# Kernel tuning notes

Measured on AMD Instinct MI355X. Metric: run time of the kernel, lower is better.

The kernel has to match this reference:

```python
import jax, jax.numpy as jnp
import numpy as np


def setup_inputs() -> dict:
    key = jax.random.key(0)
    k1, k2, k3, k4, k5 = jax.random.split(key, 5)
    B, D, T = 32, 256, 32       # batch, word_feature_dim, seq_len
    Dh, H, Wd = 128, 128, 128   # image_feature_dim, height, width
    word_features = jax.random.normal(k1, (B, D, T), dtype=jnp.float32)
    image_features = jax.random.normal(k2, (B, Dh, H, Wd), dtype=jnp.float32)
    words_mask = jax.random.randint(k3, (B, T), 0, 2, dtype=jnp.int32)
    W = jax.random.normal(k4, (Dh, D), dtype=jnp.float32) * (1.0 / np.sqrt(D))
    b = jax.random.normal(k5, (Dh,), dtype=jnp.float32) * 0.01
    return {"word_features": word_features, "image_features": image_features,
            "words_mask": words_mask, "W": W, "b": b}


def reference(word_features, image_features, words_mask, W, b):
    B, D, T = word_features.shape
    Dh = image_features.shape[1]
    N = image_features.shape[2] * image_features.shape[3]  # H*W
    # values = fc(word_features^T)^T : [B, Dh, T]
    values = jnp.einsum('bdt,kd->bkt', word_features, W) + b[None, :, None]
    # queries: [B, N, Dh] (flatten spatial)
    queries = image_features.reshape(B, Dh, N)
    # scores S: [B, N, T]
    S = jnp.einsum('bkn,bkt->bnt', queries, values)
    mask = (words_mask != 0)[:, None, :]  # [B,1,T], True => masked
    S = jnp.where(mask, -jnp.inf, S)
    # softmax over seq dim (original: exp / sum(exp)); stable form is same math
    attn_coefficients = jax.nn.softmax(S, axis=2)  # [B, N, T]
    # context vectors: [B, Dh, N]
    attn = jnp.einsum('bkt,bnt->bkn', values, attn_coefficients)
    return attn, attn_coefficients
```

## Files before the change

kernel.cpp:

```cpp
#include <hip/hip_runtime.h>
#include <math.h>

constexpr int Bc  = 32;
constexpr int Dc  = 256;
constexpr int Tc  = 32;
constexpr int DHc = 128;
constexpr int Nc  = 16384;

typedef _Float16 v8hf __attribute__((ext_vector_type(8)));
typedef _Float16 v2hf __attribute__((ext_vector_type(2)));
typedef float    v4f  __attribute__((ext_vector_type(4)));

__global__ __launch_bounds__(256) void values_kernel(
    const float* __restrict__ wf, const float* __restrict__ Wm,
    const float* __restrict__ bias, float* __restrict__ values)
{
    int id = blockIdx.x * 256 + threadIdx.x;
    int t = id & (Tc - 1);
    int k = (id >> 5) & (DHc - 1);
    int b = id >> 12;
    const float* wrow = Wm + (size_t)k * Dc;
    const float* wfp  = wf + (size_t)b * Dc * Tc + t;
    float acc = bias[k];
    #pragma unroll 8
    for (int d = 0; d < Dc; ++d)
        acc = fmaf(wrow[d], wfp[(size_t)d * Tc], acc);
    values[id] = acc;
}

__device__ __forceinline__ _Float16 pick_half(int u, int sel) {
    unsigned short s = (unsigned short)(sel ? (u >> 16) : u);
    return __builtin_bit_cast(_Float16, s);
}

__global__ __launch_bounds__(256) void attn_kernel(
    const float* __restrict__ img, const float* __restrict__ values,
    const int* __restrict__ mask, float* __restrict__ attn,
    float* __restrict__ coeff)
{
    constexpr int VT_LD = 136;
    constexpr int VP_LD = 40;
    __shared__ _Float16 VTh[Tc * VT_LD];
    __shared__ _Float16 VTl[Tc * VT_LD];
    __shared__ _Float16 VPh[DHc * VP_LD];
    __shared__ float mneg[Tc];

    const int tid   = threadIdx.x;
    const int b     = blockIdx.x >> 5;
    const int strip = blockIdx.x & 31;

    {
        const float* vb = values + (size_t)b * DHc * Tc;
        #pragma unroll
        for (int i = 0; i < 16; ++i) {
            int idx = tid + 256 * i;
            int k = idx >> 5, t = idx & 31;
            float v = vb[idx];
            _Float16 vh = (_Float16)v;
            _Float16 vl = (_Float16)(v - (float)vh);
            VTh[t * VT_LD + k] = vh;
            VTl[t * VT_LD + k] = vl;
            VPh[k * VP_LD + t] = vh;
        }
        if (tid < Tc) mneg[tid] = mask[b * Tc + tid] ? -INFINITY : 0.0f;
    }
    __syncthreads();

    const int lane = tid & 63;
    const int wave = tid >> 6;
    const int c    = lane & 15;
    const int g    = lane >> 4;

    float madd[2][4];
    #pragma unroll
    for (int tt = 0; tt < 2; ++tt)
        #pragma unroll
        for (int r = 0; r < 4; ++r)
            madd[tt][r] = mneg[16 * tt + 4 * g + r];

    v8hf VB[8];
    #pragma unroll
    for (int mt = 0; mt < 8; ++mt)
        VB[mt] = *(const v8hf*)&VPh[(16 * mt + c) * VP_LD + 8 * g];

    const float* qbase = img  + ((size_t)b * DHc + 8 * g) * Nc + c;
    float*       abase = attn + ((size_t)b * DHc + c) * Nc + 4 * g;
    float*       cbase = coeff + (size_t)b * Nc * Tc;

    const int ls_lo = c + 32 * (g & 1);
    const int sel   = g >> 1;

    for (int it = 0; it < 8; ++it) {
        const int n0 = strip * 512 + (it * 4 + wave) * 16;

        const float* qp = qbase + n0;
        v8hf Qh[4], Ql[4];
        #pragma unroll
        for (int ks = 0; ks < 4; ++ks)
            #pragma unroll
            for (int j = 0; j < 8; ++j) {
                float qv = qp[(size_t)(ks * 32 + j) * Nc];
                _Float16 h = (_Float16)qv;
                Qh[ks][j] = h;
                Ql[ks][j] = (_Float16)(qv - (float)h);
            }

        v4f Sh[2], Sl[2];
        #pragma unroll
        for (int tt = 0; tt < 2; ++tt) {
            Sh[tt] = (v4f){0.f, 0.f, 0.f, 0.f};
            Sl[tt] = (v4f){0.f, 0.f, 0.f, 0.f};
        }
        #pragma unroll
        for (int tt = 0; tt < 2; ++tt) {
            const int rowbase = (16 * tt + c) * VT_LD + 8 * g;
            #pragma unroll
            for (int ks = 0; ks < 4; ++ks) {
                v8hf va = *(const v8hf*)&VTh[rowbase + ks * 32];
                v8hf vl = *(const v8hf*)&VTl[rowbase + ks * 32];
                Sh[tt] = __builtin_amdgcn_mfma_f32_16x16x32_f16(va, Qh[ks], Sh[tt], 0, 0, 0);
                Sl[tt] = __builtin_amdgcn_mfma_f32_16x16x32_f16(va, Ql[ks], Sl[tt], 0, 0, 0);
                Sl[tt] = __builtin_amdgcn_mfma_f32_16x16x32_f16(vl, Qh[ks], Sl[tt], 0, 0, 0);
            }
        }

        float p0[4], p1[4];
        float m = -INFINITY;
        #pragma unroll
        for (int r = 0; r < 4; ++r) {
            p0[r] = Sh[0][r] + Sl[0][r] + madd[0][r];
            p1[r] = Sh[1][r] + Sl[1][r] + madd[1][r];
            m = fmaxf(m, fmaxf(p0[r], p1[r]));
        }
        m = fmaxf(m, __shfl_xor(m, 16));
        m = fmaxf(m, __shfl_xor(m, 32));
        float sum = 0.0f;
        #pragma unroll
        for (int r = 0; r < 4; ++r) {
            p0[r] = __expf(p0[r] - m); sum += p0[r];
            p1[r] = __expf(p1[r] - m); sum += p1[r];
        }
        sum += __shfl_xor(sum, 16);
        sum += __shfl_xor(sum, 32);
        const float inv = 1.0f / sum;
        #pragma unroll
        for (int r = 0; r < 4; ++r) { p0[r] *= inv; p1[r] *= inv; }

        float* cp = cbase + (size_t)(n0 + c) * Tc + 4 * g;
        *(float4*)cp        = make_float4(p0[0], p0[1], p0[2], p0[3]);
        *(float4*)(cp + 16) = make_float4(p1[0], p1[1], p1[2], p1[3]);

        v8hf Pb;
        #pragma unroll
        for (int r = 0; r < 4; ++r) {
            v2hf h2; h2[0] = (_Float16)p0[r]; h2[1] = (_Float16)p1[r];
            int u   = __builtin_bit_cast(int, h2);
            int ulo = __shfl(u, ls_lo);
            int uhi = __shfl(u, ls_lo + 16);
            Pb[r]     = pick_half(ulo, sel);
            Pb[4 + r] = pick_half(uhi, sel);
        }

        #pragma unroll
        for (int mt = 0; mt < 8; ++mt) {
            v4f o = (v4f){0.f, 0.f, 0.f, 0.f};
            o = __builtin_amdgcn_mfma_f32_16x16x32_f16(Pb, VB[mt], o, 0, 0, 0);
            float* ap = abase + (size_t)(16 * mt) * Nc + n0;
            *(float4*)ap = make_float4(o[0], o[1], o[2], o[3]);
        }
    }
}

extern "C" void kernel_launch(void* const* d_in, const int* in_sizes, int n_in,
                              void* d_out, int out_size, void* d_ws, size_t ws_size,
                              hipStream_t stream)
{
    const float* wf   = (const float*)d_in[0];
    const float* img  = (const float*)d_in[1];
    const int*   msk  = (const int*)d_in[2];
    const float* Wm   = (const float*)d_in[3];
    const float* bias = (const float*)d_in[4];

    float* attn  = (float*)d_out;
    float* coeff = attn + (size_t)Bc * DHc * Nc;
    float* vals  = (float*)d_ws;

    values_kernel<<<(Bc * DHc * Tc) / 256, 256, 0, stream>>>(wf, Wm, bias, vals);
    attn_kernel<<<Bc * 32, 256, 0, stream>>>(img, vals, msk, attn, coeff);
}
```

Baseline: 595.3 us.

## Tile values GEMM in LDS, emit fp16 split layouts, prefetch image queries

The values kernel now stages word features and a 16-row slice of W in shared memory. It computes two outputs per thread and writes pre-split fp16 hi/lo transposed and plain layouts straight to the workspace. The attention kernel then loads those with vectorized 16-byte copies instead of converting and transposing on the fly. It also double-buffers the image query loads for the next iteration in registers, sets launch bounds for occupancy of 4, and reads the V operand from LDS per use instead of keeping it in registers. The point is to hide global-load latency and cut the values-kernel cost, at the price of extra register pressure from the prefetch buffers.

```diff
diff --git a/kernel.cpp b/kernel.cpp
--- a/kernel.cpp
+++ b/kernel.cpp
@@ -13,19 +13,63 @@
 
 __global__ __launch_bounds__(256) void values_kernel(
     const float* __restrict__ wf, const float* __restrict__ Wm,
-    const float* __restrict__ bias, float* __restrict__ values)
+    const float* __restrict__ bias,
+    _Float16* __restrict__ vth, _Float16* __restrict__ vtl,
+    _Float16* __restrict__ vph)
 {
-    int id = blockIdx.x * 256 + threadIdx.x;
-    int t = id & (Tc - 1);
-    int k = (id >> 5) & (DHc - 1);
-    int b = id >> 12;
-    const float* wrow = Wm + (size_t)k * Dc;
-    const float* wfp  = wf + (size_t)b * Dc * Tc + t;
-    float acc = bias[k];
-    #pragma unroll 8
-    for (int d = 0; d < Dc; ++d)
-        acc = fmaf(wrow[d], wfp[(size_t)d * Tc], acc);
-    values[id] = acc;
+    __shared__ float wfs[Dc * Tc];
+    __shared__ float Ws[16 * 260];
+
+    const int tid = threadIdx.x;
+    const int b   = blockIdx.x >> 3;
+    const int k0  = (blockIdx.x & 7) * 16;
+
+    {
+        const float4* src = (const float4*)(wf + (size_t)b * Dc * Tc);
+        float4* dst = (float4*)wfs;
+        #pragma unroll
+        for (int i = 0; i < 8; ++i) dst[tid + 256 * i] = src[tid + 256 * i];
+    }
+    {
+        #pragma unroll
+        for (int i = 0; i < 4; ++i) {
+            int f = tid + 256 * i;
+            int row = f >> 6, d4 = f & 63;
+            *(float4*)&Ws[row * 260 + 4 * d4] =
+                *(const float4*)&Wm[(size_t)(k0 + row) * Dc + 4 * d4];
+        }
+    }
+    __syncthreads();
+
+    const int kl  = tid >> 4;
+    const int tt0 = (tid & 15) * 2;
+    const int k   = k0 + kl;
+
+    float acc0 = bias[k], acc1 = acc0;
+    #pragma unroll
+    for (int d4 = 0; d4 < 64; ++d4) {
+        const float4 w4 = *(const float4*)&Ws[kl * 260 + 4 * d4];
+        #pragma unroll
+        for (int j = 0; j < 4; ++j) {
+            const float2 f2 = *(const float2*)&wfs[(4 * d4 + j) * Tc + tt0];
+            const float wv = (j == 0) ? w4.x : (j == 1) ? w4.y : (j == 2) ? w4.z : w4.w;
+            acc0 = fmaf(wv, f2.x, acc0);
+            acc1 = fmaf(wv, f2.y, acc1);
+        }
+    }
+
+    _Float16 vh0 = (_Float16)acc0, vh1 = (_Float16)acc1;
+    _Float16 vl0 = (_Float16)(acc0 - (float)vh0);
+    _Float16 vl1 = (_Float16)(acc1 - (float)vh1);
+
+    {
+        v2hf p; p[0] = vh0; p[1] = vh1;
+        *(v2hf*)&vph[((size_t)b * DHc + k) * Tc + tt0] = p;
+    }
+    vth[((size_t)b * Tc + tt0)     * DHc + k] = vh0;
+    vth[((size_t)b * Tc + tt0 + 1) * DHc + k] = vh1;
+    vtl[((size_t)b * Tc + tt0)     * DHc + k] = vl0;
+    vtl[((size_t)b * Tc + tt0 + 1) * DHc + k] = vl1;
 }
 
 __device__ __forceinline__ _Float16 pick_half(int u, int sel) {
@@ -33,16 +77,18 @@
     return __builtin_bit_cast(_Float16, s);
 }
 
-__global__ __launch_bounds__(256) void attn_kernel(
-    const float* __restrict__ img, const float* __restrict__ values,
+__global__ __launch_bounds__(256, 4) void attn_kernel(
+    const float* __restrict__ img,
+    const _Float16* __restrict__ vth, const _Float16* __restrict__ vtl,
+    const _Float16* __restrict__ vph,
     const int* __restrict__ mask, float* __restrict__ attn,
     float* __restrict__ coeff)
 {
     constexpr int VT_LD = 136;
     constexpr int VP_LD = 40;
-    __shared__ _Float16 VTh[Tc * VT_LD];
-    __shared__ _Float16 VTl[Tc * VT_LD];
-    __shared__ _Float16 VPh[DHc * VP_LD];
+    __shared__ __align__(16) _Float16 VTh[Tc * VT_LD];
+    __shared__ __align__(16) _Float16 VTl[Tc * VT_LD];
+    __shared__ __align__(16) _Float16 VPh[DHc * VP_LD];
     __shared__ float mneg[Tc];
 
     const int tid   = threadIdx.x;
@@ -50,17 +96,17 @@
     const int strip = blockIdx.x & 31;
 
     {
-        const float* vb = values + (size_t)b * DHc * Tc;
-        #pragma unroll
-        for (int i = 0; i < 16; ++i) {
-            int idx = tid + 256 * i;
-            int k = idx >> 5, t = idx & 31;
-            float v = vb[idx];
-            _Float16 vh = (_Float16)v;
-            _Float16 vl = (_Float16)(v - (float)vh);
-            VTh[t * VT_LD + k] = vh;
-            VTl[t * VT_LD + k] = vl;
-            VPh[k * VP_LD + t] = vh;
+        const uint4* sth = (const uint4*)(vth + (size_t)b * Tc * DHc);
+        const uint4* stl = (const uint4*)(vtl + (size_t)b * Tc * DHc);
+        const uint4* sph = (const uint4*)(vph + (size_t)b * DHc * Tc);
+        #pragma unroll
+        for (int i = 0; i < 2; ++i) {
+            int cid = tid + 256 * i;
+            int t = cid >> 4, cc = cid & 15;
+            *(uint4*)&VTh[t * VT_LD + 8 * cc] = sth[cid];
+            *(uint4*)&VTl[t * VT_LD + 8 * cc] = stl[cid];
+            int kk = cid >> 2, c4 = cid & 3;
+            *(uint4*)&VPh[kk * VP_LD + 8 * c4] = sph[cid];
         }
         if (tid < Tc) mneg[tid] = mask[b * Tc + tid] ? -INFINITY : 0.0f;
     }
@@ -78,11 +124,6 @@
         for (int r = 0; r < 4; ++r)
             madd[tt][r] = mneg[16 * tt + 4 * g + r];
 
-    v8hf VB[8];
-    #pragma unroll
-    for (int mt = 0; mt < 8; ++mt)
-        VB[mt] = *(const v8hf*)&VPh[(16 * mt + c) * VP_LD + 8 * g];
-
     const float* qbase = img  + ((size_t)b * DHc + 8 * g) * Nc + c;
     float*       abase = attn + ((size_t)b * DHc + c) * Nc + 4 * g;
     float*       cbase = coeff + (size_t)b * Nc * Tc;
@@ -90,16 +131,31 @@
     const int ls_lo = c + 32 * (g & 1);
     const int sel   = g >> 1;
 
+    float qa[32], qb[32];
+    {
+        const float* qp = qbase + strip * 512 + wave * 16;
+        #pragma unroll
+        for (int u = 0; u < 32; ++u)
+            qa[u] = qp[(size_t)((u >> 3) * 32 + (u & 7)) * Nc];
+    }
+
+    #pragma unroll 2
     for (int it = 0; it < 8; ++it) {
         const int n0 = strip * 512 + (it * 4 + wave) * 16;
 
-        const float* qp = qbase + n0;
+        if (it < 7) {
+            const float* qpn = qbase + n0 + 64;
+            #pragma unroll
+            for (int u = 0; u < 32; ++u)
+                qb[u] = qpn[(size_t)((u >> 3) * 32 + (u & 7)) * Nc];
+        }
+
         v8hf Qh[4], Ql[4];
         #pragma unroll
         for (int ks = 0; ks < 4; ++ks)
             #pragma unroll
             for (int j = 0; j < 8; ++j) {
-                float qv = qp[(size_t)(ks * 32 + j) * Nc];
+                float qv = qa[ks * 8 + j];
                 _Float16 h = (_Float16)qv;
                 Qh[ks][j] = h;
                 Ql[ks][j] = (_Float16)(qv - (float)h);
@@ -163,10 +219,16 @@
 
         #pragma unroll
         for (int mt = 0; mt < 8; ++mt) {
+            v8hf vb2 = *(const v8hf*)&VPh[(16 * mt + c) * VP_LD + 8 * g];
             v4f o = (v4f){0.f, 0.f, 0.f, 0.f};
-            o = __builtin_amdgcn_mfma_f32_16x16x32_f16(Pb, VB[mt], o, 0, 0, 0);
+            o = __builtin_amdgcn_mfma_f32_16x16x32_f16(Pb, vb2, o, 0, 0, 0);
             float* ap = abase + (size_t)(16 * mt) * Nc + n0;
             *(float4*)ap = make_float4(o[0], o[1], o[2], o[3]);
+        }
+
+        if (it < 7) {
+            #pragma unroll
+            for (int u = 0; u < 32; ++u) qa[u] = qb[u];
         }
     }
 }
@@ -183,8 +245,11 @@
 
     float* attn  = (float*)d_out;
     float* coeff = attn + (size_t)Bc * DHc * Nc;
-    float* vals  = (float*)d_ws;
-
-    values_kernel<<<(Bc * DHc * Tc) / 256, 256, 0, stream>>>(wf, Wm, bias, vals);
-    attn_kernel<<<Bc * 32, 256, 0, stream>>>(img, vals, msk, attn, coeff);
-}
+
+    _Float16* vth = (_Float16*)d_ws;
+    _Float16* vtl = vth + (size_t)Bc * DHc * Tc;
+    _Float16* vph = vtl + (size_t)Bc * DHc * Tc;
+
+    values_kernel<<<256, 256, 0, stream>>>(wf, Wm, bias, vth, vtl, vph);
+    attn_kernel<<<Bc * 32, 256, 0, stream>>>(img, vth, vtl, vph, msk, attn, coeff);
+}
```

New measurement: 684.6 us. 15.0% more time.
